# Performance work log

Measured on AMD Instinct MI355X. Metric: run time of the kernel, lower is better.

Reference implementation:

```python
import jax, jax.numpy as jnp
import numpy as np

B, C, H, W = 8, 256, 48, 48
CK = 64  # C // k
WSCALE = 0.3 / np.sqrt(C)  # keep exp(QK^T) finite (original has no 1/sqrt(d) scaling)


def conv1x1(x, w, b):
    # x: (B,C,H,W), w: (O,C,1,1), b: (O,) -> (B,O,H,W)
    return jnp.einsum('bchw,oc->bohw', x, w[:, :, 0, 0]) + b[None, :, None, None]


def setup_inputs() -> dict:
    key = jax.random.key(0)
    ks = jax.random.split(key, 6)
    x = jax.random.normal(ks[0], (B, C, H, W), dtype=jnp.float32)
    qw = jax.random.normal(ks[1], (CK, C, 1, 1), dtype=jnp.float32) * WSCALE
    kw = jax.random.normal(ks[2], (CK, C, 1, 1), dtype=jnp.float32) * WSCALE
    vw = jax.random.normal(ks[3], (C, C, 1, 1), dtype=jnp.float32) * (1.0 / np.sqrt(C))
    gw = jax.random.normal(ks[4], (C, C, 1, 1), dtype=jnp.float32) * (1.0 / np.sqrt(C))
    zk = jnp.zeros((CK,), dtype=jnp.float32)
    zc = jnp.zeros((C,), dtype=jnp.float32)
    return {
        'x': x,
        'query_weight': qw, 'query_bias': zk,
        'key_weight': kw, 'key_bias': zk,
        'value_weight': vw, 'value_bias': zc,
        'gamma_weight': gw, 'gamma_bias': zc,
        'k': 4,
    }


def reference(x, query_weight, query_bias, key_weight, key_bias,
              value_weight, value_bias, gamma_weight, gamma_bias, k):
    b, c, h, w = x.shape
    n = h * w
    q = conv1x1(x, query_weight, query_bias).reshape(b, -1, n)   # (B,Ck,N)
    kk = conv1x1(x, key_weight, key_bias).reshape(b, -1, n)      # (B,Ck,N)
    # energy[b,i,j] = q_i . k_j  (queries on rows, no sqrt(d) scaling)
    energy = jnp.einsum('bci,bcj->bij', q, kk)                   # (B,N,N)
    energy = jnp.exp(energy)
    energy = energy / jnp.sum(energy, axis=2, keepdims=True)     # unnormalized-softmax over keys
    v = conv1x1(x, value_weight, value_bias).reshape(b, c, n)    # (B,C,N)
    # out[b,c,j] = sum_i v[b,c,i] * energy[b,i,j]  (faithful to torch.bmm(V, energy))
    out = jnp.einsum('bci,bij->bcj', v, energy).reshape(b, c, h, w)
    out = conv1x1(out, gamma_weight, gamma_bias)
    return out
```

## Files before the change

kernel.cpp:

```cpp
#include <hip/hip_runtime.h>

#define BATCH 8
#define CIN   256
#define NPIX  2304
#define CKD   64
#define NIT   (NPIX / 16)
#define NIC   (NPIX / 32)
#define NJB   (NPIX / 64)

typedef _Float16 f16;
typedef __attribute__((ext_vector_type(4))) _Float16 f16x4;
typedef __attribute__((ext_vector_type(8))) _Float16 f16x8;
typedef __attribute__((ext_vector_type(4))) float    f32x4;


__global__ __launch_bounds__(256) void cast_w(
    const float* __restrict__ qw, const float* __restrict__ kw,
    const float* __restrict__ vw, const float* __restrict__ gw,
    f16* __restrict__ Wqk, f16* __restrict__ Wv, f16* __restrict__ Wg)
{
    int idx = (blockIdx.x * 256 + threadIdx.x) * 4;
    const float* src;
    f16* dst;
    if (idx < 16384)      { src = qw + idx;           dst = Wqk + idx; }
    else if (idx < 32768) { src = kw + (idx - 16384); dst = Wqk + idx; }
    else if (idx < 98304) { src = vw + (idx - 32768); dst = Wv + (idx - 32768); }
    else                  { src = gw + (idx - 98304); dst = Wg + (idx - 98304); }
    float4 v = *(const float4*)src;
    f16x4 h = { (f16)v.x, (f16)v.y, (f16)v.z, (f16)v.w };
    *(f16x4*)dst = h;
}

__global__ __launch_bounds__(256) void cast_xT(
    const float* __restrict__ x, f16* __restrict__ xT)
{
    __shared__ float s[64][65];
    const int t = threadIdx.x;
    const int n0 = blockIdx.x * 64, c0 = blockIdx.y * 64, b = blockIdx.z;
    const float* xb = x + ((size_t)b * CIN + c0) * NPIX + n0;

    const int cl = t >> 4, ng = (t & 15) * 4;
    #pragma unroll
    for (int p = 0; p < 4; ++p) {
        float4 v = *(const float4*)(xb + (size_t)(cl + 16 * p) * NPIX + ng);
        s[cl + 16 * p][ng + 0] = v.x;
        s[cl + 16 * p][ng + 1] = v.y;
        s[cl + 16 * p][ng + 2] = v.z;
        s[cl + 16 * p][ng + 3] = v.w;
    }
    __syncthreads();
    const int nl = t >> 2, cs = (t & 3) * 16;
    f16 h[16];
    #pragma unroll
    for (int j = 0; j < 16; ++j) h[j] = (f16)s[cs + j][nl];
    f16* gp = &xT[((size_t)b * NPIX + n0 + nl) * CIN + c0 + cs];
    *(f16x8*)gp       = *(f16x8*)&h[0];
    *(f16x8*)(gp + 8) = *(f16x8*)&h[8];
}

__global__ __launch_bounds__(256) void qk_conv_mfma(
    const f16* __restrict__ xT, const f16* __restrict__ Wqk,
    const float* __restrict__ qbias, const float* __restrict__ kbias,
    f16* __restrict__ q_blk, f16* __restrict__ k_blk)
{
    __shared__ __align__(16) f16 us[32 * 136];
    const int t = threadIdx.x, w = t >> 6, lane = t & 63;
    const int quad = lane >> 4, l16 = lane & 15;
    const int wm = w & 1, wn = w >> 1;
    const int n0 = blockIdx.x * 32, b = blockIdx.y;

    const f16* bp = xT + ((size_t)b * NPIX + n0 + 16 * wn + l16) * CIN;
    const f16* ap = Wqk + (size_t)(64 * wm + l16) * CIN;

    f32x4 acc[4];
    #pragma unroll
    for (int mt = 0; mt < 4; ++mt) acc[mt] = (f32x4){0.f, 0.f, 0.f, 0.f};

    #pragma unroll
    for (int kk = 0; kk < CIN; kk += 32) {
        f16x8 bf = *(const f16x8*)(bp + kk + quad * 8);
        #pragma unroll
        for (int mt = 0; mt < 4; ++mt) {
            f16x8 af = *(const f16x8*)(ap + (size_t)mt * 16 * CIN + kk + quad * 8);
            acc[mt] = __builtin_amdgcn_mfma_f32_16x16x32_f16(af, bf, acc[mt], 0, 0, 0);
        }
    }
    const float* bias = wm ? kbias - 64 : qbias;
    #pragma unroll
    for (int mt = 0; mt < 4; ++mt) {
        int ob = 64 * wm + 16 * mt + quad * 4;
        #pragma unroll
        for (int r = 0; r < 4; ++r)
            us[(16 * wn + l16) * 136 + ob + r] = (f16)(acc[mt][r] + bias[ob + r]);
    }
    __syncthreads();
    {
        int ks2 = t >> 7, nt = (t >> 6) & 1, ln = t & 63;
        const f16* usr = &us[(nt * 16 + (ln & 15)) * 136 + ks2 * 32 + (ln >> 4) * 8];
        size_t base = (((size_t)b * NIT + (n0 >> 4) + nt) * 2 + ks2) * 512 + ln * 8;
        *(f16x8*)&q_blk[base] = *(const f16x8*)(usr);
        *(f16x8*)&k_blk[base] = *(const f16x8*)(usr + 64);
    }
}

#define ESL 136
__global__ __launch_bounds__(256) void energy_S(
    const f16* __restrict__ q_blk, const f16* __restrict__ k_blk,
    float* __restrict__ Pred)
{
    __shared__ __align__(16) f16 es[64 * ESL];
    __shared__ float red2[2][128];
    const int t    = threadIdx.x;
    const int w    = t >> 6, lane = t & 63;
    const int quad = lane >> 4, l16 = lane & 15;
    const int j0 = blockIdx.x * 64, i0 = blockIdx.y * 128, b = blockIdx.z;
    const size_t ln8 = (size_t)lane * 8;
    const f16* qb = q_blk + (size_t)b * NIT * 2 * 512 + ln8;

    f32x4 acc[8];
    #pragma unroll
    for (int mt = 0; mt < 8; ++mt) acc[mt] = (f32x4){0.f, 0.f, 0.f, 0.f};

    #pragma unroll
    for (int ks = 0; ks < 2; ++ks) {
        f16x8 bf = *(const f16x8*)(k_blk +
            (((size_t)b * NIT + (j0 >> 4) + w) * 2 + ks) * 512 + ln8);
        #pragma unroll
        for (int mt = 0; mt < 8; ++mt) {
            f16x8 af = *(const f16x8*)(qb + ((size_t)((i0 >> 4) + mt) * 2 + ks) * 512);
            acc[mt] = __builtin_amdgcn_mfma_f32_16x16x32_f16(af, bf, acc[mt], 0, 0, 0);
        }
    }

    #pragma unroll
    for (int mt = 0; mt < 8; ++mt) {
        f16x4 h = { (f16)__expf(acc[mt][0]), (f16)__expf(acc[mt][1]),
                    (f16)__expf(acc[mt][2]), (f16)__expf(acc[mt][3]) };
        *(f16x4*)&es[(16 * w + l16) * ESL + 16 * mt + quad * 4] = h;
    }
    __syncthreads();
    {
        int i = t & 127, jq = t >> 7;
        float s = 0.f;
        #pragma unroll
        for (int jj = 0; jj < 32; ++jj)
            s += (float)es[(jq * 32 + jj) * ESL + i];
        red2[jq][i] = s;
    }
    __syncthreads();
    if (t < 128)
        Pred[((size_t)blockIdx.x * BATCH + b) * NPIX + i0 + t] =
            red2[0][t] + red2[1][t];
}

__global__ __launch_bounds__(256) void reduce_S(
    const float* __restrict__ Pred, float* __restrict__ S)
{
    const size_t BN = (size_t)BATCH * NPIX;
    size_t idx = (size_t)blockIdx.x * 256 + threadIdx.x;
    float s = 0.f;
    #pragma unroll
    for (int jb = 0; jb < NJB; ++jb)
        s += Pred[(size_t)jb * BN + idx];
    S[idx] = s;
}

__global__ __launch_bounds__(256) void v_conv_mfma(
    const f16* __restrict__ xT, const f16* __restrict__ Wv,
    const float* __restrict__ vbias, const float* __restrict__ S,
    f16* __restrict__ u_blk)
{
    __shared__ __align__(16) f16 smem[9216];
    f16* As = smem;
    f16* Bs = smem + 128 * 40;
    f16* us = smem;
    const int t = threadIdx.x, w = t >> 6, lane = t & 63;
    const int quad = lane >> 4, l16 = lane & 15;
    const int wm = w & 1, wn = w >> 1;
    const int i0 = blockIdx.x * 64, c0 = blockIdx.y * 128, b = blockIdx.z;
    const int sub = t >> 2, le = t & 3;
    const f16* srcA = Wv + (size_t)(c0 + sub) * CIN + le * 8;
    const f16* srcB = xT + ((size_t)b * NPIX + i0 + sub) * CIN + le * 8;
    const int ldsw = sub * 40 + le * 8;

    f32x4 acc[4][2];
    #pragma unroll
    for (int mt = 0; mt < 4; ++mt)
        #pragma unroll
        for (int nt = 0; nt < 2; ++nt)
            acc[mt][nt] = (f32x4){0.f, 0.f, 0.f, 0.f};

    for (int kk = 0; kk < CIN; kk += 32) {
        f16x8 ta0 = *(const f16x8*)(srcA + kk);
        f16x8 ta1 = *(const f16x8*)(srcA + (size_t)64 * CIN + kk);
        f16x8 tb0 = *(const f16x8*)(srcB + kk);
        __syncthreads();
        *(f16x8*)&As[ldsw]           = ta0;
        *(f16x8*)&As[64 * 40 + ldsw] = ta1;
        *(f16x8*)&Bs[ldsw]           = tb0;
        __syncthreads();
        f16x8 af[4], bf[2];
        #pragma unroll
        for (int mt = 0; mt < 4; ++mt)
            af[mt] = *(const f16x8*)&As[(64 * wm + 16 * mt + l16) * 40 + quad * 8];
        #pragma unroll
        for (int nt = 0; nt < 2; ++nt)
            bf[nt] = *(const f16x8*)&Bs[(32 * wn + 16 * nt + l16) * 40 + quad * 8];
        #pragma unroll
        for (int mt = 0; mt < 4; ++mt)
            #pragma unroll
            for (int nt = 0; nt < 2; ++nt)
                acc[mt][nt] = __builtin_amdgcn_mfma_f32_16x16x32_f16(
                    af[mt], bf[nt], acc[mt][nt], 0, 0, 0);
    }

    __syncthreads();
    #pragma unroll
    for (int nt = 0; nt < 2; ++nt) {
        int i = 32 * wn + 16 * nt + l16;
        float is = 1.0f / S[(size_t)b * NPIX + i0 + i];
        #pragma unroll
        for (int mt = 0; mt < 4; ++mt)
            #pragma unroll
            for (int r = 0; r < 4; ++r) {
                int c = 64 * wm + 16 * mt + quad * 4 + r;
                us[c * 72 + i] = (f16)((acc[mt][nt][r] + vbias[c0 + c]) * is);
            }
    }
    __syncthreads();
    #pragma unroll
    for (int p = 0; p < 4; ++p) {
        int g  = t + 256 * p;
        int ct = g >> 7, ic = (g >> 6) & 1, ln = g & 63;
        f16x8 v = *(const f16x8*)&us[(ct * 16 + (ln & 15)) * 72 + ic * 32 + (ln >> 4) * 8];
        *(f16x8*)&u_blk[(((size_t)b * 16 + (c0 >> 4) + ct) * NIC + (i0 >> 5) + ic) * 512 + ln * 8] = v;
    }
}

__global__ __launch_bounds__(512) void fused_bmm(
    const f16* __restrict__ q_blk, const f16* __restrict__ k_blk,
    const f16* __restrict__ u_blk, f16* __restrict__ o1T)
{
    __shared__ __align__(16) f16 es[2][4][512];
    const int t = threadIdx.x, w = t >> 6, lane = t & 63;
    const int quad = lane >> 4, l16 = lane & 15;
    const int j0 = blockIdx.x * 32;
    const int b = blockIdx.y;
    const size_t ln8 = (size_t)lane * 8;

    const f16* qb = q_blk + (size_t)b * NIT * 2 * 512 + ln8;
    const f16* ub = u_blk + (size_t)b * 16 * NIC * 512 + ln8;

    const int jt1 = w & 1;
    const int iw  = w >> 1;

    f16x8 kf[2];
    #pragma unroll
    for (int ks = 0; ks < 2; ++ks)
        kf[ks] = *(const f16x8*)(k_blk +
            (((size_t)b * NIT + (j0 >> 4) + jt1) * 2 + ks) * 512 + ln8);

    const int CT0 = w * 2;
    const int etile = jt1 * 2 + (iw >> 1);
    const int woff  = ((iw & 1) * 2 + (quad >> 1)) * 128 + l16 * 8 + (quad & 1) * 4;

    f32x4 acc[2][2];
    #pragma unroll
    for (int mt = 0; mt < 2; ++mt)
        #pragma unroll
        for (int jt = 0; jt < 2; ++jt)
            acc[mt][jt] = (f32x4){0.f, 0.f, 0.f, 0.f};

    for (int ic = 0; ic < NPIX / 64; ++ic) {
        const int cur = ic & 1;
        f32x4 e = (f32x4){0.f, 0.f, 0.f, 0.f};
        #pragma unroll
        for (int ks = 0; ks < 2; ++ks) {
            f16x8 af = *(const f16x8*)(qb + ((size_t)(ic * 4 + iw) * 2 + ks) * 512);
            e = __builtin_amdgcn_mfma_f32_16x16x32_f16(af, kf[ks], e, 0, 0, 0);
        }
        f16x4 h = { (f16)__expf(e[0]), (f16)__expf(e[1]),
                    (f16)__expf(e[2]), (f16)__expf(e[3]) };
        *(f16x4*)&es[cur][etile][woff] = h;
        __syncthreads();
        #pragma unroll
        for (int isub = 0; isub < 2; ++isub) {
            f16x8 af0 = *(const f16x8*)(ub + ((size_t)(CT0 + 0) * NIC + ic * 2 + isub) * 512);
            f16x8 af1 = *(const f16x8*)(ub + ((size_t)(CT0 + 1) * NIC + ic * 2 + isub) * 512);
            #pragma unroll
            for (int jt = 0; jt < 2; ++jt) {
                f16x8 bf = *(const f16x8*)&es[cur][jt * 2 + isub][ln8];
                acc[0][jt] = __builtin_amdgcn_mfma_f32_16x16x32_f16(af0, bf, acc[0][jt], 0, 0, 0);
                acc[1][jt] = __builtin_amdgcn_mfma_f32_16x16x32_f16(af1, bf, acc[1][jt], 0, 0, 0);
            }
        }
    }

    #pragma unroll
    for (int mt = 0; mt < 2; ++mt) {
        int cb = 32 * w + 16 * mt + quad * 4;
        #pragma unroll
        for (int jt = 0; jt < 2; ++jt) {
            int j = j0 + 16 * jt + l16;
            f16x4 h2 = { (f16)acc[mt][jt][0], (f16)acc[mt][jt][1],
                         (f16)acc[mt][jt][2], (f16)acc[mt][jt][3] };
            *(f16x4*)&o1T[((size_t)b * NPIX + j) * CIN + cb] = h2;
        }
    }
}

__global__ __launch_bounds__(256) void gamma_conv_mfma(
    const f16* __restrict__ o1T, const f16* __restrict__ Wg,
    const float* __restrict__ gbias, float* __restrict__ out)
{
    __shared__ __align__(16) f16 As[128 * 40];
    __shared__ __align__(16) f16 Bs[64 * 40];
    const int t = threadIdx.x, w = t >> 6, lane = t & 63;
    const int quad = lane >> 4, l16 = lane & 15;
    const int wm = w & 1, wn = w >> 1;
    const int j0 = blockIdx.x * 64, o0 = blockIdx.y * 128, b = blockIdx.z;
    const int sub = t >> 2, le = t & 3;
    const f16* srcA = Wg + (size_t)(o0 + sub) * CIN + le * 8;
    const f16* srcB = o1T + ((size_t)b * NPIX + j0 + sub) * CIN + le * 8;
    const int ldsw = sub * 40 + le * 8;

    f32x4 acc[4][2];
    #pragma unroll
    for (int mt = 0; mt < 4; ++mt)
        #pragma unroll
        for (int nt = 0; nt < 2; ++nt)
            acc[mt][nt] = (f32x4){0.f, 0.f, 0.f, 0.f};

    for (int kk = 0; kk < CIN; kk += 32) {
        f16x8 ta0 = *(const f16x8*)(srcA + kk);
        f16x8 ta1 = *(const f16x8*)(srcA + (size_t)64 * CIN + kk);
        f16x8 tb0 = *(const f16x8*)(srcB + kk);
        __syncthreads();
        *(f16x8*)&As[ldsw]           = ta0;
        *(f16x8*)&As[64 * 40 + ldsw] = ta1;
        *(f16x8*)&Bs[ldsw]           = tb0;
        __syncthreads();
        f16x8 af[4], bf[2];
        #pragma unroll
        for (int mt = 0; mt < 4; ++mt)
            af[mt] = *(const f16x8*)&As[(64 * wm + 16 * mt + l16) * 40 + quad * 8];
        #pragma unroll
        for (int nt = 0; nt < 2; ++nt)
            bf[nt] = *(const f16x8*)&Bs[(32 * wn + 16 * nt + l16) * 40 + quad * 8];
        #pragma unroll
        for (int mt = 0; mt < 4; ++mt)
            #pragma unroll
            for (int nt = 0; nt < 2; ++nt)
                acc[mt][nt] = __builtin_amdgcn_mfma_f32_16x16x32_f16(
                    af[mt], bf[nt], acc[mt][nt], 0, 0, 0);
    }

    #pragma unroll
    for (int mt = 0; mt < 4; ++mt)
        #pragma unroll
        for (int r = 0; r < 4; ++r) {
            int o = o0 + 64 * wm + 16 * mt + quad * 4 + r;
            float bv = gbias[o];
            #pragma unroll
            for (int nt = 0; nt < 2; ++nt) {
                int j = j0 + 32 * wn + 16 * nt + l16;
                out[((size_t)b * CIN + o) * NPIX + j] = acc[mt][nt][r] + bv;
            }
        }
}

extern "C" void kernel_launch(void* const* d_in, const int* in_sizes, int n_in,
                              void* d_out, int out_size, void* d_ws, size_t ws_size,
                              hipStream_t stream) {
    const float* x   = (const float*)d_in[0];
    const float* qw  = (const float*)d_in[1];
    const float* qbv = (const float*)d_in[2];
    const float* kw  = (const float*)d_in[3];
    const float* kbv = (const float*)d_in[4];
    const float* vw  = (const float*)d_in[5];
    const float* vbv = (const float*)d_in[6];
    const float* gw  = (const float*)d_in[7];
    const float* gbv = (const float*)d_in[8];
    float* out = (float*)d_out;

    const size_t BCN  = (size_t)BATCH * CIN * NPIX;
    const size_t BN   = (size_t)BATCH * NPIX;
    const size_t BNCK = (size_t)BATCH * NPIX * CKD;

    f16* q_blk = (f16*)d_ws;
    f16* k_blk = q_blk + BNCK;
    f16* u_blk = k_blk + BNCK;
    f16* xT    = u_blk + BCN;
    f16* o1T   = xT + BCN;
    f16* Wqk   = o1T + BCN;
    f16* Wv    = Wqk + 128 * 256;
    f16* Wg    = Wv + 256 * 256;
    float* S   = (float*)(Wg + 256 * 256);
    float* Pred= S + BN;

    cast_w<<<160, 256, 0, stream>>>(qw, kw, vw, gw, Wqk, Wv, Wg);
    cast_xT<<<dim3(NPIX / 64, CIN / 64, BATCH), 256, 0, stream>>>(x, xT);
    qk_conv_mfma<<<dim3(NPIX / 32, BATCH), 256, 0, stream>>>(xT, Wqk, qbv, kbv, q_blk, k_blk);
    energy_S<<<dim3(NPIX / 64, NPIX / 128, BATCH), 256, 0, stream>>>(q_blk, k_blk, Pred);
    reduce_S<<<(int)(BN / 256), 256, 0, stream>>>(Pred, S);
    v_conv_mfma<<<dim3(NPIX / 64, CIN / 128, BATCH), 256, 0, stream>>>(xT, Wv, vbv, S, u_blk);
    fused_bmm<<<dim3(NPIX / 32, BATCH), 512, 0, stream>>>(q_blk, k_blk, u_blk, o1T);
    gamma_conv_mfma<<<dim3(NPIX / 64, CIN / 128, BATCH), 256, 0, stream>>>(o1T, Wg, gbv, out);
}
```

Measured before the change: 198.4 us.

## Widen fused_bmm tile to 64 key columns per block and interleave batches

Each fused_bmm block now computes 64 output columns instead of 32. Every u-operand fragment loaded from global memory therefore feeds twice as many MFMAs, which halves total u_blk traffic. The grid is flattened, with the batch index taken from the low bits of the block ID, so batches are interleaved across neighbouring blocks, and launch bounds request more resident blocks. The trade-off is fewer blocks (288 vs 576), doubled accumulator and energy-tile LDS usage, and higher register pressure.

```diff
diff --git a/kernel.cpp b/kernel.cpp
--- a/kernel.cpp
+++ b/kernel.cpp
@@ -237,58 +237,67 @@
     }
 }
 
-__global__ __launch_bounds__(512) void fused_bmm(
+__global__ __launch_bounds__(512, 4) void fused_bmm(
     const f16* __restrict__ q_blk, const f16* __restrict__ k_blk,
     const f16* __restrict__ u_blk, f16* __restrict__ o1T)
 {
-    __shared__ __align__(16) f16 es[2][4][512];
+    __shared__ __align__(16) f16 es[2][8][512];
     const int t = threadIdx.x, w = t >> 6, lane = t & 63;
     const int quad = lane >> 4, l16 = lane & 15;
-    const int j0 = blockIdx.x * 32;
-    const int b = blockIdx.y;
+    const int bid = blockIdx.x;
+    const int b  = bid & 7;
+    const int j0 = (bid >> 3) * 64;
     const size_t ln8 = (size_t)lane * 8;
 
     const f16* qb = q_blk + (size_t)b * NIT * 2 * 512 + ln8;
     const f16* ub = u_blk + (size_t)b * 16 * NIC * 512 + ln8;
 
-    const int jt1 = w & 1;
-    const int iw  = w >> 1;
-
-    f16x8 kf[2];
-    #pragma unroll
-    for (int ks = 0; ks < 2; ++ks)
-        kf[ks] = *(const f16x8*)(k_blk +
-            (((size_t)b * NIT + (j0 >> 4) + jt1) * 2 + ks) * 512 + ln8);
+    const int iw = w >> 1;
+    const int jh = w & 1;
+
+    f16x8 kf[2][2];
+    #pragma unroll
+    for (int jj = 0; jj < 2; ++jj)
+        #pragma unroll
+        for (int ks = 0; ks < 2; ++ks)
+            kf[jj][ks] = *(const f16x8*)(k_blk +
+                (((size_t)b * NIT + (j0 >> 4) + jh + 2 * jj) * 2 + ks) * 512 + ln8);
 
     const int CT0 = w * 2;
-    const int etile = jt1 * 2 + (iw >> 1);
-    const int woff  = ((iw & 1) * 2 + (quad >> 1)) * 128 + l16 * 8 + (quad & 1) * 4;
-
-    f32x4 acc[2][2];
+    const int woff = ((iw & 1) * 2 + (quad >> 1)) * 128 + l16 * 8 + (quad & 1) * 4;
+    const int et0 = jh * 2 + (iw >> 1);
+    const int et1 = (jh + 2) * 2 + (iw >> 1);
+
+    f32x4 acc[2][4];
     #pragma unroll
     for (int mt = 0; mt < 2; ++mt)
         #pragma unroll
-        for (int jt = 0; jt < 2; ++jt)
+        for (int jt = 0; jt < 4; ++jt)
             acc[mt][jt] = (f32x4){0.f, 0.f, 0.f, 0.f};
 
     for (int ic = 0; ic < NPIX / 64; ++ic) {
         const int cur = ic & 1;
-        f32x4 e = (f32x4){0.f, 0.f, 0.f, 0.f};
+        f32x4 e0 = (f32x4){0.f, 0.f, 0.f, 0.f};
+        f32x4 e1 = (f32x4){0.f, 0.f, 0.f, 0.f};
         #pragma unroll
         for (int ks = 0; ks < 2; ++ks) {
             f16x8 af = *(const f16x8*)(qb + ((size_t)(ic * 4 + iw) * 2 + ks) * 512);
-            e = __builtin_amdgcn_mfma_f32_16x16x32_f16(af, kf[ks], e, 0, 0, 0);
-        }
-        f16x4 h = { (f16)__expf(e[0]), (f16)__expf(e[1]),
-                    (f16)__expf(e[2]), (f16)__expf(e[3]) };
-        *(f16x4*)&es[cur][etile][woff] = h;
+            e0 = __builtin_amdgcn_mfma_f32_16x16x32_f16(af, kf[0][ks], e0, 0, 0, 0);
+            e1 = __builtin_amdgcn_mfma_f32_16x16x32_f16(af, kf[1][ks], e1, 0, 0, 0);
+        }
+        f16x4 h0 = { (f16)__expf(e0[0]), (f16)__expf(e0[1]),
+                     (f16)__expf(e0[2]), (f16)__expf(e0[3]) };
+        f16x4 h1 = { (f16)__expf(e1[0]), (f16)__expf(e1[1]),
+                     (f16)__expf(e1[2]), (f16)__expf(e1[3]) };
+        *(f16x4*)&es[cur][et0][woff] = h0;
+        *(f16x4*)&es[cur][et1][woff] = h1;
         __syncthreads();
         #pragma unroll
         for (int isub = 0; isub < 2; ++isub) {
             f16x8 af0 = *(const f16x8*)(ub + ((size_t)(CT0 + 0) * NIC + ic * 2 + isub) * 512);
             f16x8 af1 = *(const f16x8*)(ub + ((size_t)(CT0 + 1) * NIC + ic * 2 + isub) * 512);
             #pragma unroll
-            for (int jt = 0; jt < 2; ++jt) {
+            for (int jt = 0; jt < 4; ++jt) {
                 f16x8 bf = *(const f16x8*)&es[cur][jt * 2 + isub][ln8];
                 acc[0][jt] = __builtin_amdgcn_mfma_f32_16x16x32_f16(af0, bf, acc[0][jt], 0, 0, 0);
                 acc[1][jt] = __builtin_amdgcn_mfma_f32_16x16x32_f16(af1, bf, acc[1][jt], 0, 0, 0);
@@ -300,7 +309,7 @@
     for (int mt = 0; mt < 2; ++mt) {
         int cb = 32 * w + 16 * mt + quad * 4;
         #pragma unroll
-        for (int jt = 0; jt < 2; ++jt) {
+        for (int jt = 0; jt < 4; ++jt) {
             int j = j0 + 16 * jt + l16;
             f16x4 h2 = { (f16)acc[mt][jt][0], (f16)acc[mt][jt][1],
                          (f16)acc[mt][jt][2], (f16)acc[mt][jt][3] };
@@ -404,6 +413,6 @@
     energy_S<<<dim3(NPIX / 64, NPIX / 128, BATCH), 256, 0, stream>>>(q_blk, k_blk, Pred);
     reduce_S<<<(int)(BN / 256), 256, 0, stream>>>(Pred, S);
     v_conv_mfma<<<dim3(NPIX / 64, CIN / 128, BATCH), 256, 0, stream>>>(xT, Wv, vbv, S, u_blk);
-    fused_bmm<<<dim3(NPIX / 32, BATCH), 512, 0, stream>>>(q_blk, k_blk, u_blk, o1T);
+    fused_bmm<<<NJB * BATCH, 512, 0, stream>>>(q_blk, k_blk, u_blk, o1T);
     gamma_conv_mfma<<<dim3(NPIX / 64, CIN / 128, BATCH), 256, 0, stream>>>(o1T, Wg, gbv, out);
 }
```

After: 202.8 us. 2.2% more time.
